# Performance work log

Measured on AMD Instinct MI355X. Metric: run time of the kernel, lower is better.

## Reference

```python
import jax, jax.numpy as jnp
import numpy as np

EMBED_DIM = 256
NUM_HEADS = 8
HEAD_DIM = 32
BIAS_HIDDEN = 64
LN_EPS = 1e-5


def setup_inputs() -> dict:
    key = jax.random.key(0)
    ks = jax.random.split(key, 12)
    B, N = 2, 1024
    inner = NUM_HEADS * HEAD_DIM  # 256
    inp = {
        'x': jax.random.normal(ks[0], (B, N, EMBED_DIM), dtype=jnp.float32),
        'coords': jax.random.normal(ks[1], (B, N, 2), dtype=jnp.float32),
        'velocities': jax.random.normal(ks[2], (B, N, 2), dtype=jnp.float32),
        # LayerNorm params
        'ln_g': jnp.ones((EMBED_DIM,), jnp.float32),
        'ln_b': jnp.zeros((EMBED_DIM,), jnp.float32),
        # qkv projection (no bias)
        'w_qkv': jax.random.normal(ks[3], (EMBED_DIM, 3 * inner), dtype=jnp.float32) * (EMBED_DIM ** -0.5),
        # output projection
        'w_o': jax.random.normal(ks[4], (inner, EMBED_DIM), dtype=jnp.float32) * (inner ** -0.5),
        'b_o': jnp.zeros((EMBED_DIM,), jnp.float32),
        # relational bias MLP: Linear(5,64) -> GELU -> Linear(64, num_heads)
        'w1': jax.random.normal(ks[5], (5, BIAS_HIDDEN), dtype=jnp.float32) * (5 ** -0.5),
        'b1': jnp.zeros((BIAS_HIDDEN,), jnp.float32),
        'w2': jax.random.normal(ks[6], (BIAS_HIDDEN, NUM_HEADS), dtype=jnp.float32) * (BIAS_HIDDEN ** -0.5),
        'b2': jnp.zeros((NUM_HEADS,), jnp.float32),
    }
    return inp


def _rope_sin_cos(n, dim):
    half = dim // 2  # rotary applied over half pairs
    inv_freq = 1.0 / (10000.0 ** (jnp.arange(0, half, dtype=jnp.float32) / half))
    freqs = jnp.arange(n, dtype=jnp.float32)[:, None] * inv_freq[None, :]  # [n, half]
    return jnp.sin(freqs), jnp.cos(freqs)


def _apply_rope(t, sin, cos):
    d = t.shape[-1]
    t1, t2 = t[..., : d // 2], t[..., d // 2 :]
    return jnp.concatenate([t1 * cos - t2 * sin, t2 * cos + t1 * sin], axis=-1)


def reference(x, coords, velocities, ln_g, ln_b, w_qkv, w_o, b_o, w1, b1, w2, b2):
    b, n, _ = x.shape
    # LayerNorm
    mu = jnp.mean(x, axis=-1, keepdims=True)
    var = jnp.mean((x - mu) ** 2, axis=-1, keepdims=True)
    h = (x - mu) / jnp.sqrt(var + LN_EPS) * ln_g + ln_b
    # qkv
    qkv = h @ w_qkv  # [b, n, 3*inner]
    inner = NUM_HEADS * HEAD_DIM
    q, k, v = jnp.split(qkv, 3, axis=-1)
    reshape_heads = lambda t: t.reshape(b, n, NUM_HEADS, HEAD_DIM).transpose(0, 2, 1, 3)
    q, k, v = reshape_heads(q), reshape_heads(k), reshape_heads(v)  # [b,h,n,d]
    sin, cos = _rope_sin_cos(n, HEAD_DIM)  # [n, d//2], broadcast over b,h
    q = _apply_rope(q, sin, cos)
    k = _apply_rope(k, sin, cos)
    scale = HEAD_DIM ** -0.5
    scores = jnp.einsum('bhnd,bhmd->bhnm', q, k) * scale  # [b,h,n,n] fp32
    # relational bias: pairwise MLP over [dx(2), |dx|(1), dv(2)]
    dx = coords[:, :, None, :] - coords[:, None, :, :]        # [b,n,n,2]
    dist = jnp.linalg.norm(dx, axis=-1, keepdims=True)        # [b,n,n,1]
    dv = velocities[:, :, None, :] - velocities[:, None, :, :]
    feats = jnp.concatenate([dx, dist, dv], axis=-1)          # [b,n,n,5]
    hid = jax.nn.gelu(feats @ w1 + b1, approximate=False)     # [b,n,n,64]
    rel = (hid @ w2 + b2).transpose(0, 3, 1, 2)               # [b,h,n,n]
    scores = scores + rel
    probs = jax.nn.softmax(scores, axis=-1)
    probs = jnp.nan_to_num(probs, nan=0.0)
    out = jnp.einsum('bhnm,bhmd->bhnd', probs, v)
    out = out.transpose(0, 2, 1, 3).reshape(b, n, inner)
    return out @ w_o + b_o
```

## Files before the change

kernel.cpp:

```cpp
#include <hip/hip_runtime.h>
#include <hip/hip_bf16.h>
#include <hip/hip_fp16.h>
#include <math.h>
#include <string.h>

typedef _Float16 half8 __attribute__((ext_vector_type(8)));
typedef _Float16 half4 __attribute__((ext_vector_type(4)));
typedef float floatx4 __attribute__((ext_vector_type(4)));
typedef float floatx16 __attribute__((ext_vector_type(16)));

#if defined(__has_builtin) && __has_builtin(__builtin_amdgcn_mfma_f32_16x16x16f16)
#define MFMA_PV(a, b, c) __builtin_amdgcn_mfma_f32_16x16x16f16((a), (b), (c), 0, 0, 0)
#else
__device__ __forceinline__ floatx4 mfma_pv_asm(half4 a, half4 b, floatx4 c) {
  floatx4 d;
  asm volatile("v_mfma_f32_16x16x16_f16 %0, %1, %2, %3"
               : "=v"(d) : "v"(a), "v"(b), "v"(c));
  return d;
}
#define MFMA_PV(a, b, c) mfma_pv_asm((a), (b), (c))
#endif

__device__ __forceinline__ floatx16 MFMA_S1(half4 a, half4 b, floatx16 c) {
#if defined(__has_builtin) && __has_builtin(__builtin_amdgcn_mfma_f32_32x32x8f16)
  return __builtin_amdgcn_mfma_f32_32x32x8f16(a, b, c, 0, 0, 0);
#else
  floatx16 d;
  asm volatile("v_mfma_f32_32x32x8_f16 %0, %1, %2, %3"
               : "=v"(d) : "v"(a), "v"(b), "v"(c));
  return d;
#endif
}

__device__ __forceinline__ floatx16 MFMA_S2(half8 a, half8 b, floatx16 c) {
#if defined(__has_builtin) && __has_builtin(__builtin_amdgcn_mfma_f32_32x32x16_f16)
  return __builtin_amdgcn_mfma_f32_32x32x16_f16(a, b, c, 0, 0, 0);
#else
  floatx16 d;
  asm volatile("v_mfma_f32_32x32x16_f16 %0, %1, %2, %3"
               : "=v"(d) : "v"(a), "v"(b), "v"(c));
  return d;
#endif
}

__device__ __forceinline__ float gelu_exact(float z) {
  return 0.5f * z * (1.0f + erff(z * 0.70710678118654752f));
}
__device__ __forceinline__ unsigned int packh2(float a, float b) {
  __half2 h = __halves2half2(__float2half_rn(a), __float2half_rn(b));
  unsigned int u;
  memcpy(&u, &h, 4);
  return u;
}

__global__ __launch_bounds__(256) void prep_kernel(
    const float* __restrict__ x, const float* __restrict__ g,
    const float* __restrict__ bv, __half* __restrict__ h16,
    const float* __restrict__ w_qkv, const float* __restrict__ w_o,
    const float* __restrict__ w1, const float* __restrict__ b1,
    const float* __restrict__ w2,
    __half* __restrict__ wqT, __half* __restrict__ woT,
    unsigned int* __restrict__ gtabu, uint2* __restrict__ A1g,
    uint4* __restrict__ A2g) {
  int t = threadIdx.x;
  if (blockIdx.x < 2048) {
    int row = blockIdx.x;
    float v = x[(size_t)row * 256 + t];
    float s = v, q = v * v;
#pragma unroll
    for (int o = 32; o > 0; o >>= 1) {
      s += __shfl_xor(s, o);
      q += __shfl_xor(q, o);
    }
    __shared__ float ss[4], qq[4];
    int w = t >> 6, l = t & 63;
    if (l == 0) { ss[w] = s; qq[w] = q; }
    __syncthreads();
    s = ss[0] + ss[1] + ss[2] + ss[3];
    q = qq[0] + qq[1] + qq[2] + qq[3];
    float mu = s * (1.f / 256.f);
    float var = q * (1.f / 256.f) - mu * mu;
    float inv = rsqrtf(var + 1e-5f);
    h16[(size_t)row * 256 + t] = __float2half_rn((v - mu) * inv * g[t] + bv[t]);
    return;
  }
  int bx = blockIdx.x - 2048;
  if (bx < 768) {
    wqT[(size_t)bx * 256 + t] = __float2half_rn(w_qkv[(size_t)t * 768 + bx]);
  } else if (bx < 1024) {
    int n = bx - 768;
    woT[(size_t)n * 256 + t] = __float2half_rn(w_o[(size_t)t * 256 + n]);
  } else if (bx == 1024) {
#pragma unroll
    for (int s = 0; s < 8; s++) {
      int e = t * 8 + s;
      float z = -16.f + (float)e * (1.f / 64.f);
      float g0 = gelu_exact(z);
      float g1 = gelu_exact(z + (1.f / 64.f));
      gtabu[e] = packh2(g0, g1 - g0);
    }
  } else {
    if (t < 128) {
      int hb = t >> 6, l = t & 63;
      int hid = hb * 32 + (l & 31);
      float v[4];
#pragma unroll
      for (int e = 0; e < 4; e++) {
        int k = (l >> 5) * 4 + e;
        v[e] = (k < 5) ? w1[k * 64 + hid] : ((k == 5) ? b1[hid] : 0.f);
      }
      A1g[t] = make_uint2(packh2(v[0], v[1]), packh2(v[2], v[3]));
    }
    {
      int c = t >> 6, l = t & 63;
      int row = l & 31;
      int lh = l >> 5;
      float v[8];
#pragma unroll
      for (int e = 0; e < 8; e++) {
        int hid = c * 16 + (e & 3) + 8 * (e >> 2) + 4 * lh;
        v[e] = (row < 8) ? w2[hid * 8 + row] : 0.f;
      }
      A2g[t] = make_uint4(packh2(v[0], v[1]), packh2(v[2], v[3]),
                          packh2(v[4], v[5]), packh2(v[6], v[7]));
    }
  }
}

__global__ __launch_bounds__(256) void qkv_rope(
    const __half* __restrict__ h16, const __half* __restrict__ wqT,
    __half* __restrict__ qo, __half* __restrict__ ko, __half* __restrict__ vo) {
  int wave = blockIdx.x * 4 + (threadIdx.x >> 6);
  int mt = wave / 24, nt = wave - mt * 24;
  int l = threadIdx.x & 63;
  int c31 = l & 31, kg = l >> 5;
  int m0 = mt * 32, n0 = nt * 32;
  floatx16 acc0 = {0.f}, acc1 = {0.f};
  const _Float16* ap = (const _Float16*)h16 + (size_t)(m0 + c31) * 256 + kg * 8;
  const _Float16* bp = (const _Float16*)wqT + (size_t)(n0 + c31) * 256 + kg * 8;
  for (int k0 = 0; k0 < 256; k0 += 32) {
    half8 a0 = *(const half8*)(ap + k0);
    half8 b0 = *(const half8*)(bp + k0);
    half8 a1 = *(const half8*)(ap + k0 + 16);
    half8 b1 = *(const half8*)(bp + k0 + 16);
    acc0 = MFMA_S2(a0, b0, acc0);
    acc1 = MFMA_S2(a1, b1, acc1);
  }
  floatx16 acc = acc0 + acc1;

  if (nt < 16) {
    __half* dst = (nt < 8) ? qo : ko;
    int hh = nt & 7;
    int f = c31 & 15;
    float inv_freq = exp2f((float)f * -0.8304820237218407f);
#pragma unroll
    for (int r = 0; r < 16; r++) {
      float part = __shfl_xor(acc[r], 16);
      int m = m0 + (r & 3) + 8 * (r >> 2) + 4 * kg;
      int nseq = m & 1023, bb = m >> 10;
      float sn, cs;
      __sincosf((float)nseq * inv_freq, &sn, &cs);
      float out = (c31 < 16) ? (acc[r] * cs - part * sn)
                             : (acc[r] * cs + part * sn);
      dst[((size_t)(bb * 8 + hh) * 1024 + nseq) * 32 + c31] = __float2half_rn(out);
    }
  } else {
    int hh = nt - 16;
#pragma unroll
    for (int r = 0; r < 16; r++) {
      int m = m0 + (r & 3) + 8 * (r >> 2) + 4 * kg;
      int nseq = m & 1023, bb = m >> 10;
      vo[((size_t)(bb * 8 + hh) * 1024 + nseq) * 32 + c31] = __float2half_rn(acc[r]);
    }
  }
}

__global__ __launch_bounds__(256) void gemm16(
    const __half* __restrict__ A16, const __half* __restrict__ BT16,
    const float* __restrict__ bias, float* __restrict__ C,
    int ntn, int N, int K) {
  int wave = blockIdx.x * 4 + (threadIdx.x >> 6);
  int mt = wave / ntn, nt = wave - mt * ntn;
  int l = threadIdx.x & 63;
  int lg = l >> 4, li = l & 15;
  int m0 = mt * 16, n0 = nt * 16;
  floatx4 acc0 = {0.f, 0.f, 0.f, 0.f};
  floatx4 acc1 = {0.f, 0.f, 0.f, 0.f};
  const _Float16* ap = (const _Float16*)A16 + (size_t)(m0 + li) * K + 8 * lg;
  const _Float16* bp = (const _Float16*)BT16 + (size_t)(n0 + li) * K + 8 * lg;
  for (int k0 = 0; k0 < K; k0 += 64) {
    half8 a0 = *(const half8*)(ap + k0);
    half8 b0 = *(const half8*)(bp + k0);
    half8 a1 = *(const half8*)(ap + k0 + 32);
    half8 b1 = *(const half8*)(bp + k0 + 32);
    acc0 = __builtin_amdgcn_mfma_f32_16x16x32_f16(a0, b0, acc0, 0, 0, 0);
    acc1 = __builtin_amdgcn_mfma_f32_16x16x32_f16(a1, b1, acc1, 0, 0, 0);
  }
  float bb = bias ? bias[n0 + li] : 0.f;
#pragma unroll
  for (int r = 0; r < 4; r++) {
    C[(size_t)(m0 + 4 * lg + r) * N + n0 + li] = acc0[r] + acc1[r] + bb;
  }
}

__device__ __forceinline__ _Float16 gelu_tab16(float z, const unsigned int* gt) {
  float tf = __builtin_amdgcn_fmed3f(fmaf(z, 64.f, 1024.f), 0.f, 2047.f);
  float fr = __builtin_amdgcn_fractf(tf);
  unsigned int e = gt[(unsigned int)tf];
  union { unsigned int u; _Float16 h[2]; } cv;
  cv.u = e;
  return (_Float16)(cv.h[0] + (_Float16)fr * cv.h[1]);
}

__global__ __launch_bounds__(512) void fused_attn(
    const __half* __restrict__ qh, const __half* __restrict__ kh,
    const __half* __restrict__ vh,
    const float* __restrict__ coords, const float* __restrict__ vels,
    const unsigned int* __restrict__ gtabu, const uint2* __restrict__ A1g,
    const uint4* __restrict__ A2g, const float* __restrict__ b2,
    float* __restrict__ Opart, float* __restrict__ ml) {
  __shared__ unsigned int gtab[2048];
  __shared__ __half relS[8][64][18];
  const int t = threadIdx.x;
  for (int e = t; e < 2048; e += 512) gtab[e] = gtabu[e];

  const int js = blockIdx.x & 7;
  const int it = (blockIdx.x >> 3) & 63;
  const int b  = blockIdx.x >> 9;
  const int h  = t >> 6;
  const int lane = t & 63;
  const int lg = lane >> 4, li16 = lane & 15;
  const int li = lane & 31, lh = lane >> 5;
  const int i0 = it * 16;
  const size_t bh = (size_t)(b * 8 + h) * 1024;
  const float scale = 0.17677669529663687f;

  float b2v0 = b2[4 * lh + 0], b2v1 = b2[4 * lh + 1];
  float b2v2 = b2[4 * lh + 2], b2v3 = b2[4 * lh + 3];

  const half8 qf = *(const half8*)((const _Float16*)qh + (bh + i0 + li16) * 32 + 8 * lg);
  floatx4 accLo = {0.f, 0.f, 0.f, 0.f};
  floatx4 accHi = {0.f, 0.f, 0.f, 0.f};
  float m_run = -3.0e38f, l_run = 0.f;

  __syncthreads();

  for (int chunk = 0; chunk < 2; chunk++) {
    const int jt = js * 128 + chunk * 64;
    {
      uint2 a1u0 = A1g[lane], a1u1 = A1g[64 + lane];
      uint4 a2u0 = A2g[lane], a2u1 = A2g[64 + lane];
      uint4 a2u2 = A2g[128 + lane], a2u3 = A2g[192 + lane];
#pragma unroll
      for (int tt = 0; tt < 4; tt++) {
        const int i_loc = 2 * h + (tt >> 1);
        const int jsub = tt & 1;
        const int i = i0 + i_loc;
        const int j = jt + jsub * 32 + li;
        float2 ci = *(const float2*)&coords[(size_t)(b * 1024 + i) * 2];
        float2 vi = *(const float2*)&vels[(size_t)(b * 1024 + i) * 2];
        float2 cj = *(const float2*)&coords[(size_t)(b * 1024 + j) * 2];
        float2 vj = *(const float2*)&vels[(size_t)(b * 1024 + j) * 2];
        float dx0 = ci.x - cj.x, dx1 = ci.y - cj.y;
        float dv0 = vi.x - vj.x, dv1 = vi.y - vj.y;
        float dist = sqrtf(dx0 * dx0 + dx1 * dx1);
        half4 bf;
        bf[0] = lh ? (_Float16)dv1 : (_Float16)dx0;
        bf[1] = lh ? (_Float16)1.0f : (_Float16)dx1;
        bf[2] = lh ? (_Float16)0.0f : (_Float16)dist;
        bf[3] = lh ? (_Float16)0.0f : (_Float16)dv0;

        floatx16 zinit = {0.f};
        floatx16 acc = {0.f};
        {
          floatx16 z0 = MFMA_S1(*(half4*)&a1u0, bf, zinit);
          unsigned int u[8] __attribute__((aligned(16)));
#pragma unroll
          for (int q = 0; q < 8; q++) {
            _Float16 ga = gelu_tab16(z0[2 * q], gtab);
            _Float16 gb = gelu_tab16(z0[2 * q + 1], gtab);
            union { unsigned int uu; _Float16 hx[2]; } cv;
            cv.hx[0] = ga; cv.hx[1] = gb;
            u[q] = cv.uu;
          }
          acc = MFMA_S2(*(half8*)&a2u0, *(half8*)&u[0], acc);
          acc = MFMA_S2(*(half8*)&a2u1, *(half8*)&u[4], acc);
        }
        {
          floatx16 z1 = MFMA_S1(*(half4*)&a1u1, bf, zinit);
          unsigned int u[8] __attribute__((aligned(16)));
#pragma unroll
          for (int q = 0; q < 8; q++) {
            _Float16 ga = gelu_tab16(z1[2 * q], gtab);
            _Float16 gb = gelu_tab16(z1[2 * q + 1], gtab);
            union { unsigned int uu; _Float16 hx[2]; } cv;
            cv.hx[0] = ga; cv.hx[1] = gb;
            u[q] = cv.uu;
          }
          acc = MFMA_S2(*(half8*)&a2u2, *(half8*)&u[0], acc);
          acc = MFMA_S2(*(half8*)&a2u3, *(half8*)&u[4], acc);
        }
        const int jc = jsub * 32 + li;
        relS[4 * lh + 0][jc][i_loc] = __float2half_rn(acc[0] + b2v0);
        relS[4 * lh + 1][jc][i_loc] = __float2half_rn(acc[1] + b2v1);
        relS[4 * lh + 2][jc][i_loc] = __float2half_rn(acc[2] + b2v2);
        relS[4 * lh + 3][jc][i_loc] = __float2half_rn(acc[3] + b2v3);
      }
    }
    __syncthreads();
    {
      const _Float16* kb = (const _Float16*)kh + (bh + jt + li16) * 32 + 8 * lg;
      half8 kf0 = *(const half8*)(kb + 0 * 512);
      half8 kf1 = *(const half8*)(kb + 1 * 512);
      half8 kf2 = *(const half8*)(kb + 2 * 512);
      half8 kf3 = *(const half8*)(kb + 3 * 512);
      floatx4 zero = {0.f, 0.f, 0.f, 0.f};
      __builtin_amdgcn_s_setprio(1);
      floatx4 st0 = __builtin_amdgcn_mfma_f32_16x16x32_f16(kf0, qf, zero, 0, 0, 0);
      floatx4 st1 = __builtin_amdgcn_mfma_f32_16x16x32_f16(kf1, qf, zero, 0, 0, 0);
      floatx4 st2 = __builtin_amdgcn_mfma_f32_16x16x32_f16(kf2, qf, zero, 0, 0, 0);
      floatx4 st3 = __builtin_amdgcn_mfma_f32_16x16x32_f16(kf3, qf, zero, 0, 0, 0);
      __builtin_amdgcn_s_setprio(0);
      float s[16];
#pragma unroll
      for (int r = 0; r < 4; r++) {
        s[0 + r]  = fmaf(st0[r], scale, __half2float(relS[h][0 + 4 * lg + r][li16]));
        s[4 + r]  = fmaf(st1[r], scale, __half2float(relS[h][16 + 4 * lg + r][li16]));
        s[8 + r]  = fmaf(st2[r], scale, __half2float(relS[h][32 + 4 * lg + r][li16]));
        s[12 + r] = fmaf(st3[r], scale, __half2float(relS[h][48 + 4 * lg + r][li16]));
      }
      float tm = fmaxf(fmaxf(fmaxf(s[0], s[1]), fmaxf(s[2], s[3])),
                       fmaxf(fmaxf(s[4], s[5]), fmaxf(s[6], s[7])));
      tm = fmaxf(tm, fmaxf(fmaxf(fmaxf(s[8], s[9]), fmaxf(s[10], s[11])),
                           fmaxf(fmaxf(s[12], s[13]), fmaxf(s[14], s[15]))));
      tm = fmaxf(tm, __shfl_xor(tm, 16));
      tm = fmaxf(tm, __shfl_xor(tm, 32));
      float nm = fmaxf(m_run, tm);
      float fc = __expf(m_run - nm);
      float p[16];
#pragma unroll
      for (int e = 0; e < 16; e++) p[e] = __expf(s[e] - nm);
      float ts = ((p[0] + p[1]) + (p[2] + p[3])) + ((p[4] + p[5]) + (p[6] + p[7]));
      ts += ((p[8] + p[9]) + (p[10] + p[11])) + ((p[12] + p[13]) + (p[14] + p[15]));
      ts += __shfl_xor(ts, 16);
      ts += __shfl_xor(ts, 32);
      l_run = l_run * fc + ts;
      m_run = nm;
      float fT0 = __shfl(fc, 4 * lg + 0);
      float fT1 = __shfl(fc, 4 * lg + 1);
      float fT2 = __shfl(fc, 4 * lg + 2);
      float fT3 = __shfl(fc, 4 * lg + 3);
      accLo[0] *= fT0; accHi[0] *= fT0;
      accLo[1] *= fT1; accHi[1] *= fT1;
      accLo[2] *= fT2; accHi[2] *= fT2;
      accLo[3] *= fT3; accHi[3] *= fT3;
#pragma unroll
      for (int tt = 0; tt < 4; tt++) {
        half4 pf;
        pf[0] = (_Float16)p[4 * tt + 0];
        pf[1] = (_Float16)p[4 * tt + 1];
        pf[2] = (_Float16)p[4 * tt + 2];
        pf[3] = (_Float16)p[4 * tt + 3];
        const _Float16* vb = (const _Float16*)vh + (bh + jt + tt * 16 + 4 * lg) * 32 + li16;
        half4 vf0, vf1;
        vf0[0] = vb[0];  vf0[1] = vb[32]; vf0[2] = vb[64]; vf0[3] = vb[96];
        vf1[0] = vb[16]; vf1[1] = vb[48]; vf1[2] = vb[80]; vf1[3] = vb[112];
        __builtin_amdgcn_s_setprio(1);
        accLo = MFMA_PV(pf, vf0, accLo);
        accHi = MFMA_PV(pf, vf1, accHi);
        __builtin_amdgcn_s_setprio(0);
      }
    }
    __syncthreads();
  }
  size_t orow = (size_t)(b * 8 + js) * 1024 + i0 + 4 * lg;
#pragma unroll
  for (int r = 0; r < 4; r++) {
    float* op = Opart + (orow + r) * 256 + h * 32 + li16;
    op[0] = accLo[r];
    op[16] = accHi[r];
  }
  if (lane < 16) {
    ((float2*)ml)[((size_t)(b * 8 + js) * 1024 + i0 + lane) * 8 + h] =
        make_float2(m_run, l_run);
  }
}

__global__ __launch_bounds__(256) void combine_kernel(
    const float* __restrict__ Opart, const float* __restrict__ ml,
    __half* __restrict__ attn16) {
  int row = blockIdx.x;
  int b = row >> 10, i = row & 1023;
  int t = threadIdx.x, hh = t >> 5;
  float2 mls[8];
  float M = -1e30f;
#pragma unroll
  for (int js = 0; js < 8; js++) {
    mls[js] = ((const float2*)ml)[(((size_t)(b * 8 + js) * 1024) + i) * 8 + hh];
    M = fmaxf(M, mls[js].x);
  }
  float L = 0.f, Ov = 0.f;
#pragma unroll
  for (int js = 0; js < 8; js++) {
    float w = __expf(mls[js].x - M);
    L += mls[js].y * w;
    Ov += Opart[(((size_t)(b * 8 + js) * 1024) + i) * 256 + t] * w;
  }
  attn16[(size_t)row * 256 + t] = __float2half_rn(Ov / L);
}

extern "C" void kernel_launch(void* const* d_in, const int* in_sizes, int n_in,
                              void* d_out, int out_size, void* d_ws, size_t ws_size,
                              hipStream_t stream) {
  const float* x      = (const float*)d_in[0];
  const float* coords = (const float*)d_in[1];
  const float* vels   = (const float*)d_in[2];
  const float* ln_g   = (const float*)d_in[3];
  const float* ln_b   = (const float*)d_in[4];
  const float* w_qkv  = (const float*)d_in[5];
  const float* w_o    = (const float*)d_in[6];
  const float* b_o    = (const float*)d_in[7];
  const float* w1     = (const float*)d_in[8];
  const float* b1     = (const float*)d_in[9];
  const float* w2     = (const float*)d_in[10];
  const float* b2     = (const float*)d_in[11];
  float* out = (float*)d_out;

  char* wsb = (char*)d_ws;
  float* Opart = (float*)wsb;
  __half* wqT  = (__half*)(wsb + 16777216);
  __half* woT  = (__half*)(wsb + 17170432);
  unsigned int* gtab = (unsigned int*)(wsb + 17301504);
  uint2* A1g   = (uint2*)(wsb + 17317888);
  uint4* A2g   = (uint4*)(wsb + 17318912);
  __half* h16  = (__half*)(wsb + 17825792);
  __half* attn16 = (__half*)(wsb + 17825792);
  __half* qh   = (__half*)(wsb + 18874368);
  __half* kh   = (__half*)(wsb + 19922944);
  __half* vh   = (__half*)(wsb + 20971520);
  float* ml    = (float*)d_out;

  prep_kernel<<<3074, 256, 0, stream>>>(x, ln_g, ln_b, h16, w_qkv, w_o,
                                        w1, b1, w2, wqT, woT, gtab, A1g, A2g);
  qkv_rope<<<384, 256, 0, stream>>>(h16, wqT, qh, kh, vh);
  fused_attn<<<1024, 512, 0, stream>>>(qh, kh, vh, coords, vels, gtab,
                                       A1g, A2g, b2, Opart, ml);
  combine_kernel<<<2048, 256, 0, stream>>>(Opart, ml, attn16);
  gemm16<<<512, 256, 0, stream>>>(attn16, woT, b_o, out, 16, 256, 256);
}
```

Measured before the change: 81.26 us.

## Fuse combine with output projection and fold scale and bias into MFMA

The softmax scale is folded into Q during the RoPE epilogue, and the relational bias is loaded as the MFMA accumulator's initial value, which removes the per-element fma after the QK product. The separate combine and output-projection GEMM kernels are merged into one kernel. It stages 16 combined rows in shared memory and runs the projection from there, which removes one launch and the fp16 attn round trip through global memory. The ml buffer moves from the output buffer to workspace. The cost is that the fused kernel runs only 128 blocks, each combining 16 rows serially, so there is less parallelism.

```diff
diff --git a/kernel.cpp b/kernel.cpp
--- a/kernel.cpp
+++ b/kernel.cpp
@@ -150,6 +150,7 @@
 
   if (nt < 16) {
     __half* dst = (nt < 8) ? qo : ko;
+    float qscale = (nt < 8) ? 0.17677669529663687f : 1.0f;
     int hh = nt & 7;
     int f = c31 & 15;
     float inv_freq = exp2f((float)f * -0.8304820237218407f);
@@ -162,7 +163,8 @@
       __sincosf((float)nseq * inv_freq, &sn, &cs);
       float out = (c31 < 16) ? (acc[r] * cs - part * sn)
                              : (acc[r] * cs + part * sn);
-      dst[((size_t)(bb * 8 + hh) * 1024 + nseq) * 32 + c31] = __float2half_rn(out);
+      dst[((size_t)(bb * 8 + hh) * 1024 + nseq) * 32 + c31] =
+          __float2half_rn(out * qscale);
     }
   } else {
     int hh = nt - 16;
@@ -172,34 +174,6 @@
       int nseq = m & 1023, bb = m >> 10;
       vo[((size_t)(bb * 8 + hh) * 1024 + nseq) * 32 + c31] = __float2half_rn(acc[r]);
     }
-  }
-}
-
-__global__ __launch_bounds__(256) void gemm16(
-    const __half* __restrict__ A16, const __half* __restrict__ BT16,
-    const float* __restrict__ bias, float* __restrict__ C,
-    int ntn, int N, int K) {
-  int wave = blockIdx.x * 4 + (threadIdx.x >> 6);
-  int mt = wave / ntn, nt = wave - mt * ntn;
-  int l = threadIdx.x & 63;
-  int lg = l >> 4, li = l & 15;
-  int m0 = mt * 16, n0 = nt * 16;
-  floatx4 acc0 = {0.f, 0.f, 0.f, 0.f};
-  floatx4 acc1 = {0.f, 0.f, 0.f, 0.f};
-  const _Float16* ap = (const _Float16*)A16 + (size_t)(m0 + li) * K + 8 * lg;
-  const _Float16* bp = (const _Float16*)BT16 + (size_t)(n0 + li) * K + 8 * lg;
-  for (int k0 = 0; k0 < K; k0 += 64) {
-    half8 a0 = *(const half8*)(ap + k0);
-    half8 b0 = *(const half8*)(bp + k0);
-    half8 a1 = *(const half8*)(ap + k0 + 32);
-    half8 b1 = *(const half8*)(bp + k0 + 32);
-    acc0 = __builtin_amdgcn_mfma_f32_16x16x32_f16(a0, b0, acc0, 0, 0, 0);
-    acc1 = __builtin_amdgcn_mfma_f32_16x16x32_f16(a1, b1, acc1, 0, 0, 0);
-  }
-  float bb = bias ? bias[n0 + li] : 0.f;
-#pragma unroll
-  for (int r = 0; r < 4; r++) {
-    C[(size_t)(m0 + 4 * lg + r) * N + n0 + li] = acc0[r] + acc1[r] + bb;
   }
 }
 
@@ -233,7 +207,6 @@
   const int li = lane & 31, lh = lane >> 5;
   const int i0 = it * 16;
   const size_t bh = (size_t)(b * 8 + h) * 1024;
-  const float scale = 0.17677669529663687f;
 
   float b2v0 = b2[4 * lh + 0], b2v1 = b2[4 * lh + 1];
   float b2v2 = b2[4 * lh + 2], b2v3 = b2[4 * lh + 3];
@@ -314,20 +287,25 @@
       half8 kf1 = *(const half8*)(kb + 1 * 512);
       half8 kf2 = *(const half8*)(kb + 2 * 512);
       half8 kf3 = *(const half8*)(kb + 3 * 512);
-      floatx4 zero = {0.f, 0.f, 0.f, 0.f};
+      floatx4 c0, c1, c2, c3;
+#pragma unroll
+      for (int r = 0; r < 4; r++) {
+        c0[r] = __half2float(relS[h][0 + 4 * lg + r][li16]);
+        c1[r] = __half2float(relS[h][16 + 4 * lg + r][li16]);
+        c2[r] = __half2float(relS[h][32 + 4 * lg + r][li16]);
+        c3[r] = __half2float(relS[h][48 + 4 * lg + r][li16]);
+      }
       __builtin_amdgcn_s_setprio(1);
-      floatx4 st0 = __builtin_amdgcn_mfma_f32_16x16x32_f16(kf0, qf, zero, 0, 0, 0);
-      floatx4 st1 = __builtin_amdgcn_mfma_f32_16x16x32_f16(kf1, qf, zero, 0, 0, 0);
-      floatx4 st2 = __builtin_amdgcn_mfma_f32_16x16x32_f16(kf2, qf, zero, 0, 0, 0);
-      floatx4 st3 = __builtin_amdgcn_mfma_f32_16x16x32_f16(kf3, qf, zero, 0, 0, 0);
+      floatx4 st0 = __builtin_amdgcn_mfma_f32_16x16x32_f16(kf0, qf, c0, 0, 0, 0);
+      floatx4 st1 = __builtin_amdgcn_mfma_f32_16x16x32_f16(kf1, qf, c1, 0, 0, 0);
+      floatx4 st2 = __builtin_amdgcn_mfma_f32_16x16x32_f16(kf2, qf, c2, 0, 0, 0);
+      floatx4 st3 = __builtin_amdgcn_mfma_f32_16x16x32_f16(kf3, qf, c3, 0, 0, 0);
       __builtin_amdgcn_s_setprio(0);
       float s[16];
 #pragma unroll
       for (int r = 0; r < 4; r++) {
-        s[0 + r]  = fmaf(st0[r], scale, __half2float(relS[h][0 + 4 * lg + r][li16]));
-        s[4 + r]  = fmaf(st1[r], scale, __half2float(relS[h][16 + 4 * lg + r][li16]));
-        s[8 + r]  = fmaf(st2[r], scale, __half2float(relS[h][32 + 4 * lg + r][li16]));
-        s[12 + r] = fmaf(st3[r], scale, __half2float(relS[h][48 + 4 * lg + r][li16]));
+        s[0 + r] = st0[r]; s[4 + r] = st1[r];
+        s[8 + r] = st2[r]; s[12 + r] = st3[r];
       }
       float tm = fmaxf(fmaxf(fmaxf(s[0], s[1]), fmaxf(s[2], s[3])),
                        fmaxf(fmaxf(s[4], s[5]), fmaxf(s[6], s[7])));
@@ -386,27 +364,53 @@
   }
 }
 
-__global__ __launch_bounds__(256) void combine_kernel(
+__global__ __launch_bounds__(256) void combine_proj(
     const float* __restrict__ Opart, const float* __restrict__ ml,
-    __half* __restrict__ attn16) {
-  int row = blockIdx.x;
-  int b = row >> 10, i = row & 1023;
-  int t = threadIdx.x, hh = t >> 5;
-  float2 mls[8];
-  float M = -1e30f;
-#pragma unroll
-  for (int js = 0; js < 8; js++) {
-    mls[js] = ((const float2*)ml)[(((size_t)(b * 8 + js) * 1024) + i) * 8 + hh];
-    M = fmaxf(M, mls[js].x);
-  }
-  float L = 0.f, Ov = 0.f;
-#pragma unroll
-  for (int js = 0; js < 8; js++) {
-    float w = __expf(mls[js].x - M);
-    L += mls[js].y * w;
-    Ov += Opart[(((size_t)(b * 8 + js) * 1024) + i) * 256 + t] * w;
-  }
-  attn16[(size_t)row * 256 + t] = __float2half_rn(Ov / L);
+    const __half* __restrict__ woT, const float* __restrict__ b_o,
+    float* __restrict__ out) {
+  __shared__ _Float16 As[16][264];
+  const int r0 = blockIdx.x * 16;
+  const int t = threadIdx.x;
+  const int hh = t >> 5;
+  for (int rr = 0; rr < 16; rr++) {
+    int row = r0 + rr;
+    int b = row >> 10, i = row & 1023;
+    float2 mls[8];
+    float M = -1e30f;
+#pragma unroll
+    for (int js = 0; js < 8; js++) {
+      mls[js] = ((const float2*)ml)[(((size_t)(b * 8 + js) * 1024) + i) * 8 + hh];
+      M = fmaxf(M, mls[js].x);
+    }
+    float L = 0.f, Ov = 0.f;
+#pragma unroll
+    for (int js = 0; js < 8; js++) {
+      float w = __expf(mls[js].x - M);
+      L += mls[js].y * w;
+      Ov += Opart[(((size_t)(b * 8 + js) * 1024) + i) * 256 + t] * w;
+    }
+    As[rr][t] = (_Float16)(Ov / L);
+  }
+  __syncthreads();
+  const int wv = t >> 6, lane = t & 63;
+  const int lg = lane >> 4, li = lane & 15;
+#pragma unroll
+  for (int nt = 0; nt < 4; nt++) {
+    int n0 = (wv * 4 + nt) * 16;
+    floatx4 acc = {0.f, 0.f, 0.f, 0.f};
+    const _Float16* bp = (const _Float16*)woT + (size_t)(n0 + li) * 256 + 8 * lg;
+#pragma unroll
+    for (int k0 = 0; k0 < 256; k0 += 32) {
+      half8 af = *(const half8*)&As[li][k0 + 8 * lg];
+      half8 bf = *(const half8*)(bp + k0);
+      acc = __builtin_amdgcn_mfma_f32_16x16x32_f16(af, bf, acc, 0, 0, 0);
+    }
+    float bb = b_o[n0 + li];
+#pragma unroll
+    for (int r = 0; r < 4; r++) {
+      out[(size_t)(r0 + 4 * lg + r) * 256 + n0 + li] = acc[r] + bb;
+    }
+  }
 }
 
 extern "C" void kernel_launch(void* const* d_in, const int* in_sizes, int n_in,
@@ -434,17 +438,15 @@
   uint2* A1g   = (uint2*)(wsb + 17317888);
   uint4* A2g   = (uint4*)(wsb + 17318912);
   __half* h16  = (__half*)(wsb + 17825792);
-  __half* attn16 = (__half*)(wsb + 17825792);
   __half* qh   = (__half*)(wsb + 18874368);
   __half* kh   = (__half*)(wsb + 19922944);
   __half* vh   = (__half*)(wsb + 20971520);
-  float* ml    = (float*)d_out;
+  float* ml    = (float*)(wsb + 22020096);
 
   prep_kernel<<<3074, 256, 0, stream>>>(x, ln_g, ln_b, h16, w_qkv, w_o,
                                         w1, b1, w2, wqT, woT, gtab, A1g, A2g);
   qkv_rope<<<384, 256, 0, stream>>>(h16, wqT, qh, kh, vh);
   fused_attn<<<1024, 512, 0, stream>>>(qh, kh, vh, coords, vels, gtab,
                                        A1g, A2g, b2, Opart, ml);
-  combine_kernel<<<2048, 256, 0, stream>>>(Opart, ml, attn16);
-  gemm16<<<512, 256, 0, stream>>>(attn16, woT, b_o, out, 16, 256, 256);
-}
+  combine_proj<<<128, 256, 0, stream>>>(Opart, ml, woT, b_o, out);
+}
```

After: 87.33 us. +7.5%, slower.
